# Performance work log

Measured on AMD Instinct MI355X. Metric: run time of the kernel, lower is better.

The kernel has to match this reference:

```python
import jax, jax.numpy as jnp
import numpy as np

N, E, IN_FEATS, HID, CLS, K = 100000, 3200000, 500, 64, 40, 10
EPS = 1e-8

def _col_normalize(x):
    # column-wise L2 norm over nodes (dim=0), clamped at 1e-8
    return x / jnp.clip(jnp.linalg.norm(x, axis=0), EPS, None)

def setup_inputs() -> dict:
    key = jax.random.key(0)
    ks = jax.random.split(key, 9)
    features = jax.random.normal(ks[0], (N, IN_FEATS), jnp.float32)
    noise = jax.random.normal(ks[1], (N, HID), jnp.float32)
    edge_index = jax.random.randint(ks[2], (2, E), 0, N, dtype=jnp.int32)
    norm_A = jax.random.uniform(ks[3], (E,), jnp.float32) * 0.1  # normalized adj weights
    W1 = jax.random.normal(ks[4], (IN_FEATS, HID), jnp.float32) * (1.0 / np.sqrt(IN_FEATS))
    b1 = jax.random.normal(ks[5], (HID,), jnp.float32) * 0.01
    W2 = jax.random.normal(ks[6], (HID, CLS), jnp.float32) * (1.0 / np.sqrt(HID))
    b2 = jax.random.normal(ks[7], (CLS,), jnp.float32) * 0.01
    alpha = jax.random.normal(ks[8], (HID, K + 1), jnp.float32) * 0.1
    return {"features": features, "noise": noise, "norm_A": norm_A, "W1": W1,
            "b1": b1, "W2": W2, "b2": b2, "alpha": alpha, "edge_index": edge_index}

def reference(features, noise, norm_A, W1, b1, W2, b2, alpha, edge_index):
    # fc1 + act (dropout p=0 -> identity)
    x = jax.nn.relu(features @ W1 + b1)
    x = x + noise * 1e-5  # blank_noise = randn_like(x) * 1e-5
    h0 = _col_normalize(x)
    rst = alpha[:, 0] * h0  # broadcast per-channel over nodes
    last_h = h0
    second_last_h = jnp.zeros_like(h0)
    src, dst = edge_index[0], edge_index[1]
    for i in range(1, K + 1):
        # NormalBasisConv: h = A @ last_h (sparse), orthogonalize vs last two, column-normalize
        h = jax.ops.segment_sum(norm_A[:, None] * last_h[src], dst, num_segments=N)  # [N, HID]
        h = h - jnp.sum(h * last_h, axis=0) * last_h
        h = h - jnp.sum(h * second_last_h, axis=0) * second_last_h
        h = _col_normalize(h)
        rst = rst + alpha[:, i] * h
        second_last_h, last_h = last_h, h
    return rst @ W2 + b2
```

## Files before the change

kernel.cpp:

```cpp
#include <hip/hip_runtime.h>
#include <stdint.h>

#define N_NODES 100000
#define N_EDGES 3200000
#define IN_FEATS 500
#define HID 64
#define CLS 40
#define KHOPS 10
#define KT 32
#define NRANGE 8
#define SCAN_BS 256
#define SCAN_NBLK 391

__global__ void zero_kernel(float4* __restrict__ p, size_t n4) {
  size_t i = (size_t)blockIdx.x * blockDim.x + threadIdx.x;
  size_t stride = (size_t)gridDim.x * blockDim.x;
  float4 z = make_float4(0.f, 0.f, 0.f, 0.f);
  for (; i < n4; i += stride) p[i] = z;
}

__global__ void hist_kernel(const int* __restrict__ dst, int* __restrict__ off) {
  const int r = blockIdx.x & (NRANGE - 1);
  const int slice = blockIdx.x >> 3;
  const int nslices = gridDim.x >> 3;
  const int lo = r * (N_NODES / NRANGE);
  const int hi = lo + (N_NODES / NRANGE);
  const int per = (N_EDGES + nslices - 1) / nslices;
  const int beg = slice * per;
  int end = beg + per; if (end > N_EDGES) end = N_EDGES;
  for (int e = beg + threadIdx.x; e < end; e += blockDim.x) {
    int d = dst[e];
    if (d >= lo && d < hi) atomicAdd(&off[d + 1], 1);
  }
}

__launch_bounds__(SCAN_BS)
__global__ void scanA_kernel(const int* __restrict__ off, int* __restrict__ psum) {
  __shared__ int s[SCAN_BS];
  int b = blockIdx.x, t = threadIdx.x;
  int idx = b * SCAN_BS + t;
  s[t] = (idx < N_NODES + 1) ? off[idx] : 0;
  __syncthreads();
  for (int d = SCAN_BS / 2; d > 0; d >>= 1) {
    if (t < d) s[t] += s[t + d];
    __syncthreads();
  }
  if (t == 0) psum[b] = s[0];
}

__launch_bounds__(512)
__global__ void scanB_kernel(int* __restrict__ psum) {
  __shared__ int s[512];
  int t = threadIdx.x;
  s[t] = (t < SCAN_NBLK) ? psum[t] : 0;
  __syncthreads();
  for (int d = 1; d < 512; d <<= 1) {
    int v = (t >= d) ? s[t - d] : 0;
    __syncthreads();
    s[t] += v;
    __syncthreads();
  }
  if (t < SCAN_NBLK) psum[t] = (t == 0) ? 0 : s[t - 1];
}

__launch_bounds__(SCAN_BS)
__global__ void scanC_kernel(int* __restrict__ off, int* __restrict__ cursor,
                             const int* __restrict__ psum) {
  __shared__ int s[SCAN_BS];
  int b = blockIdx.x, t = threadIdx.x;
  int idx = b * SCAN_BS + t;
  s[t] = (idx < N_NODES + 1) ? off[idx] : 0;
  __syncthreads();
  for (int d = 1; d < SCAN_BS; d <<= 1) {
    int v = (t >= d) ? s[t - d] : 0;
    __syncthreads();
    s[t] += v;
    __syncthreads();
  }
  int run = s[t] + psum[b];
  if (idx < N_NODES + 1) {
    off[idx] = run;
    if (idx < N_NODES) cursor[idx] = run;
  }
}

__global__ void fill_kernel(const int* __restrict__ src, const int* __restrict__ dst,
                            const float* __restrict__ w, int* __restrict__ cursor,
                            int2* __restrict__ edges) {
  const int r = blockIdx.x & (NRANGE - 1);
  const int slice = blockIdx.x >> 3;
  const int nslices = gridDim.x >> 3;
  const int lo = r * (N_NODES / NRANGE);
  const int hi = lo + (N_NODES / NRANGE);
  const int per = (N_EDGES + nslices - 1) / nslices;
  const int beg = slice * per;
  int end = beg + per; if (end > N_EDGES) end = N_EDGES;
  for (int e = beg + threadIdx.x; e < end; e += blockDim.x) {
    int d = dst[e];
    if (d >= lo && d < hi) {
      int p = atomicAdd(&cursor[d], 1);
      edges[p] = make_int2(src[e], __float_as_int(w[e]));
    }
  }
}

__launch_bounds__(256)
__global__ void fc1_kernel(const float* __restrict__ F, const float* __restrict__ W1,
                           const float* __restrict__ bias1, const float* __restrict__ noise,
                           float* __restrict__ x, float* __restrict__ nn0) {
  __shared__ float Fs[KT][132];
  __shared__ float Ws[KT][64];
  __shared__ float red[64];
  const int t = threadIdx.x;
  const int tx = t & 15;
  const int ty = t >> 4;
  const int c0 = tx * 4;
  const int n0 = ty * 8;
  const int nodeBase = blockIdx.x * 128;
  const int fk = (t & 7) * 4;
  const int fn = t >> 3;
  const int wr = t >> 3;
  const int wc = (t & 7) * 8;

  float4 fr[4];
  float4 w0r, w1r;
  {
#pragma unroll
    for (int p = 0; p < 4; ++p) {
      int n = nodeBase + fn + 32 * p;
      float4 v = make_float4(0.f, 0.f, 0.f, 0.f);
      if (n < N_NODES && fk + 3 < IN_FEATS) v = *(const float4*)(F + (size_t)n * IN_FEATS + fk);
      fr[p] = v;
    }
    float4 a = make_float4(0.f, 0.f, 0.f, 0.f), b = a;
    if (wr < IN_FEATS) {
      a = *(const float4*)(W1 + (size_t)wr * HID + wc);
      b = *(const float4*)(W1 + (size_t)wr * HID + wc + 4);
    }
    w0r = a; w1r = b;
  }

  float acc[8][4];
#pragma unroll
  for (int i = 0; i < 8; ++i)
#pragma unroll
    for (int j = 0; j < 4; ++j) acc[i][j] = 0.f;

  const int NTILE = (IN_FEATS + KT - 1) / KT;
  for (int tile = 0; tile < NTILE; ++tile) {
    __syncthreads();
#pragma unroll
    for (int p = 0; p < 4; ++p) {
      Fs[fk + 0][fn + 32 * p] = fr[p].x;
      Fs[fk + 1][fn + 32 * p] = fr[p].y;
      Fs[fk + 2][fn + 32 * p] = fr[p].z;
      Fs[fk + 3][fn + 32 * p] = fr[p].w;
    }
    *(float4*)&Ws[wr][wc] = w0r;
    *(float4*)&Ws[wr][wc + 4] = w1r;
    __syncthreads();
    if (tile + 1 < NTILE) {
      const int kb = (tile + 1) * KT;
#pragma unroll
      for (int p = 0; p < 4; ++p) {
        int n = nodeBase + fn + 32 * p;
        int k = kb + fk;
        float4 v = make_float4(0.f, 0.f, 0.f, 0.f);
        if (n < N_NODES && k + 3 < IN_FEATS) v = *(const float4*)(F + (size_t)n * IN_FEATS + k);
        fr[p] = v;
      }
      int k = kb + wr;
      float4 a = make_float4(0.f, 0.f, 0.f, 0.f), b = a;
      if (k < IN_FEATS) {
        a = *(const float4*)(W1 + (size_t)k * HID + wc);
        b = *(const float4*)(W1 + (size_t)k * HID + wc + 4);
      }
      w0r = a; w1r = b;
    }
#pragma unroll 8
    for (int kk = 0; kk < KT; ++kk) {
      float4 fa = *(float4*)&Fs[kk][n0];
      float4 fb = *(float4*)&Fs[kk][n0 + 4];
      float4 wv = *(float4*)&Ws[kk][c0];
      acc[0][0] = fmaf(fa.x, wv.x, acc[0][0]); acc[0][1] = fmaf(fa.x, wv.y, acc[0][1]);
      acc[0][2] = fmaf(fa.x, wv.z, acc[0][2]); acc[0][3] = fmaf(fa.x, wv.w, acc[0][3]);
      acc[1][0] = fmaf(fa.y, wv.x, acc[1][0]); acc[1][1] = fmaf(fa.y, wv.y, acc[1][1]);
      acc[1][2] = fmaf(fa.y, wv.z, acc[1][2]); acc[1][3] = fmaf(fa.y, wv.w, acc[1][3]);
      acc[2][0] = fmaf(fa.z, wv.x, acc[2][0]); acc[2][1] = fmaf(fa.z, wv.y, acc[2][1]);
      acc[2][2] = fmaf(fa.z, wv.z, acc[2][2]); acc[2][3] = fmaf(fa.z, wv.w, acc[2][3]);
      acc[3][0] = fmaf(fa.w, wv.x, acc[3][0]); acc[3][1] = fmaf(fa.w, wv.y, acc[3][1]);
      acc[3][2] = fmaf(fa.w, wv.z, acc[3][2]); acc[3][3] = fmaf(fa.w, wv.w, acc[3][3]);
      acc[4][0] = fmaf(fb.x, wv.x, acc[4][0]); acc[4][1] = fmaf(fb.x, wv.y, acc[4][1]);
      acc[4][2] = fmaf(fb.x, wv.z, acc[4][2]); acc[4][3] = fmaf(fb.x, wv.w, acc[4][3]);
      acc[5][0] = fmaf(fb.y, wv.x, acc[5][0]); acc[5][1] = fmaf(fb.y, wv.y, acc[5][1]);
      acc[5][2] = fmaf(fb.y, wv.z, acc[5][2]); acc[5][3] = fmaf(fb.y, wv.w, acc[5][3]);
      acc[6][0] = fmaf(fb.z, wv.x, acc[6][0]); acc[6][1] = fmaf(fb.z, wv.y, acc[6][1]);
      acc[6][2] = fmaf(fb.z, wv.z, acc[6][2]); acc[6][3] = fmaf(fb.z, wv.w, acc[6][3]);
      acc[7][0] = fmaf(fb.w, wv.x, acc[7][0]); acc[7][1] = fmaf(fb.w, wv.y, acc[7][1]);
      acc[7][2] = fmaf(fb.w, wv.z, acc[7][2]); acc[7][3] = fmaf(fb.w, wv.w, acc[7][3]);
    }
  }

  float4 bb = *(const float4*)(bias1 + c0);
  float np0 = 0.f, np1 = 0.f, np2 = 0.f, np3 = 0.f;
#pragma unroll
  for (int i = 0; i < 8; ++i) {
    int n = nodeBase + n0 + i;
    if (n < N_NODES) {
      float4 nz = *(const float4*)(noise + (size_t)n * HID + c0);
      float v0 = fmaxf(acc[i][0] + bb.x, 0.f) + nz.x * 1e-5f;
      float v1 = fmaxf(acc[i][1] + bb.y, 0.f) + nz.y * 1e-5f;
      float v2 = fmaxf(acc[i][2] + bb.z, 0.f) + nz.z * 1e-5f;
      float v3 = fmaxf(acc[i][3] + bb.w, 0.f) + nz.w * 1e-5f;
      *(float4*)(x + (size_t)n * HID + c0) = make_float4(v0, v1, v2, v3);
      np0 = fmaf(v0, v0, np0); np1 = fmaf(v1, v1, np1);
      np2 = fmaf(v2, v2, np2); np3 = fmaf(v3, v3, np3);
    }
  }
  if (t < 64) red[t] = 0.f;
  __syncthreads();
  atomicAdd(&red[c0 + 0], np0); atomicAdd(&red[c0 + 1], np1);
  atomicAdd(&red[c0 + 2], np2); atomicAdd(&red[c0 + 3], np3);
  __syncthreads();
  if (t < 64) atomicAdd(&nn0[t], red[t]);
}

__launch_bounds__(256)
__global__ void spmm_kernel(const int2* __restrict__ edges, const int* __restrict__ off,
                            const float* __restrict__ lastr, const float* __restrict__ secondr,
                            const float* __restrict__ nn_l,
                            float* __restrict__ h, float* __restrict__ dslot) {
  __shared__ float red[128];
  const int t = threadIdx.x;
  const int lane = t & 63;
  const int wid = __builtin_amdgcn_readfirstlane(t >> 6);
  if (t < 128) red[t] = 0.f;
  __syncthreads();
  const float sig = 1.f / fmaxf(sqrtf(nn_l[lane]), 1e-8f);
  float d1 = 0.f, d2 = 0.f;
  const int nw = gridDim.x * 4;
  for (int n = blockIdx.x * 4 + wid; n < N_NODES; n += nw) {
    const int beg = off[n], end = off[n + 1];
    float a0 = 0.f, a1 = 0.f, a2 = 0.f, a3 = 0.f;
    float a4 = 0.f, a5 = 0.f, a6 = 0.f, a7 = 0.f;
    int j = beg;
    for (; j + 8 <= end; j += 8) {
      int2 e0 = edges[j + 0]; int2 e1 = edges[j + 1];
      int2 e2 = edges[j + 2]; int2 e3 = edges[j + 3];
      int2 e4 = edges[j + 4]; int2 e5 = edges[j + 5];
      int2 e6 = edges[j + 6]; int2 e7 = edges[j + 7];
      a0 = fmaf(__int_as_float(e0.y), lastr[(size_t)e0.x * HID + lane], a0);
      a1 = fmaf(__int_as_float(e1.y), lastr[(size_t)e1.x * HID + lane], a1);
      a2 = fmaf(__int_as_float(e2.y), lastr[(size_t)e2.x * HID + lane], a2);
      a3 = fmaf(__int_as_float(e3.y), lastr[(size_t)e3.x * HID + lane], a3);
      a4 = fmaf(__int_as_float(e4.y), lastr[(size_t)e4.x * HID + lane], a4);
      a5 = fmaf(__int_as_float(e5.y), lastr[(size_t)e5.x * HID + lane], a5);
      a6 = fmaf(__int_as_float(e6.y), lastr[(size_t)e6.x * HID + lane], a6);
      a7 = fmaf(__int_as_float(e7.y), lastr[(size_t)e7.x * HID + lane], a7);
    }
    for (; j < end; ++j) {
      int2 e = edges[j];
      a0 = fmaf(__int_as_float(e.y), lastr[(size_t)e.x * HID + lane], a0);
    }
    float acc = ((a0 + a1) + (a2 + a3)) + ((a4 + a5) + (a6 + a7));
    acc *= sig;
    size_t o = (size_t)n * HID + lane;
    float l = lastr[o], s = secondr[o];
    h[o] = acc;
    d1 = fmaf(acc, l, d1);
    d2 = fmaf(acc, s, d2);
  }
  atomicAdd(&red[lane], d1);
  atomicAdd(&red[64 + lane], d2);
  __syncthreads();
  if (t < 128) atomicAdd(&dslot[t], red[t]);
}

__launch_bounds__(256)
__global__ void passB_kernel(float4* __restrict__ h4, const float4* __restrict__ l4,
                             const float4* __restrict__ s4, float* __restrict__ dcur,
                             const float* __restrict__ nn_l, const float* __restrict__ nn_s,
                             const float* __restrict__ alpha, int prevcol, int accum,
                             float4* __restrict__ rst4) {
  __shared__ float red[64];
  int t = threadIdx.x;
  int q = t & 15;
  int c0 = q * 4;
  float4 NL = ((const float4*)nn_l)[q];
  float4 NS = ((const float4*)nn_s)[q];
  float4 D1 = ((const float4*)dcur)[q];
  float4 D2 = ((const float4*)(dcur + 64))[q];
  float4 sigl, sigs;
  sigl.x = 1.f / fmaxf(sqrtf(NL.x), 1e-8f); sigl.y = 1.f / fmaxf(sqrtf(NL.y), 1e-8f);
  sigl.z = 1.f / fmaxf(sqrtf(NL.z), 1e-8f); sigl.w = 1.f / fmaxf(sqrtf(NL.w), 1e-8f);
  sigs.x = 1.f / fmaxf(sqrtf(NS.x), 1e-8f); sigs.y = 1.f / fmaxf(sqrtf(NS.y), 1e-8f);
  sigs.z = 1.f / fmaxf(sqrtf(NS.z), 1e-8f); sigs.w = 1.f / fmaxf(sqrtf(NS.w), 1e-8f);
  float4 C1, C2, AL;
  C1.x = sigl.x * sigl.x * D1.x; C1.y = sigl.y * sigl.y * D1.y;
  C1.z = sigl.z * sigl.z * D1.z; C1.w = sigl.w * sigl.w * D1.w;
  C2.x = sigs.x * sigs.x * D2.x; C2.y = sigs.y * sigs.y * D2.y;
  C2.z = sigs.z * sigs.z * D2.z; C2.w = sigs.w * sigs.w * D2.w;
  AL.x = alpha[(size_t)(c0 + 0) * (KHOPS + 1) + prevcol] * sigl.x;
  AL.y = alpha[(size_t)(c0 + 1) * (KHOPS + 1) + prevcol] * sigl.y;
  AL.z = alpha[(size_t)(c0 + 2) * (KHOPS + 1) + prevcol] * sigl.z;
  AL.w = alpha[(size_t)(c0 + 3) * (KHOPS + 1) + prevcol] * sigl.w;
  float nx = 0.f, ny = 0.f, nz = 0.f, nw = 0.f;
  int row0 = blockIdx.x * 16 + (t >> 4);
  int rstride = gridDim.x * 16;
  for (int n = row0; n < N_NODES; n += rstride) {
    size_t idx = (size_t)n * 16 + q;
    float4 h = h4[idx];
    float4 l = l4[idx];
    float4 s = s4[idx];
    h.x -= C1.x * l.x + C2.x * s.x;
    h.y -= C1.y * l.y + C2.y * s.y;
    h.z -= C1.z * l.z + C2.z * s.z;
    h.w -= C1.w * l.w + C2.w * s.w;
    h4[idx] = h;
    nx = fmaf(h.x, h.x, nx); ny = fmaf(h.y, h.y, ny);
    nz = fmaf(h.z, h.z, nz); nw = fmaf(h.w, h.w, nw);
    float4 r;
    if (accum) {
      r = rst4[idx];
      r.x = fmaf(AL.x, l.x, r.x); r.y = fmaf(AL.y, l.y, r.y);
      r.z = fmaf(AL.z, l.z, r.z); r.w = fmaf(AL.w, l.w, r.w);
    } else {
      r.x = AL.x * l.x; r.y = AL.y * l.y; r.z = AL.z * l.z; r.w = AL.w * l.w;
    }
    rst4[idx] = r;
  }
  if (t < 64) red[t] = 0.f;
  __syncthreads();
  atomicAdd(&red[c0 + 0], nx); atomicAdd(&red[c0 + 1], ny);
  atomicAdd(&red[c0 + 2], nz); atomicAdd(&red[c0 + 3], nw);
  __syncthreads();
  if (t < 64) atomicAdd(&dcur[128 + t], red[t]);
}

__launch_bounds__(256)
__global__ void gemm2_kernel(const float* __restrict__ rst, const float* __restrict__ hK,
                             const float* __restrict__ nnK, const float* __restrict__ alpha,
                             const float* __restrict__ W2, const float* __restrict__ bias2,
                             float* __restrict__ out) {
  __shared__ float W2s[HID * CLS];
  __shared__ float R[64][65];
  __shared__ float coef[64];
  int t = threadIdx.x;
  if (t < 64) coef[t] = alpha[(size_t)t * (KHOPS + 1) + KHOPS] / fmaxf(sqrtf(nnK[t]), 1e-8f);
  for (int i = t; i < HID * CLS; i += 256) W2s[i] = W2[i];
  int nodeBase = blockIdx.x * 64;
  __syncthreads();
  for (int i = t; i < 64 * 16; i += 256) {
    int r = i >> 4, c4 = (i & 15) * 4;
    int n = nodeBase + r;
    if (n < N_NODES) {
      float4 rv = *(const float4*)(rst + (size_t)n * HID + c4);
      float4 hv = *(const float4*)(hK + (size_t)n * HID + c4);
      R[r][c4 + 0] = rv.x + coef[c4 + 0] * hv.x;
      R[r][c4 + 1] = rv.y + coef[c4 + 1] * hv.y;
      R[r][c4 + 2] = rv.z + coef[c4 + 2] * hv.z;
      R[r][c4 + 3] = rv.w + coef[c4 + 3] * hv.w;
    } else {
      R[r][c4 + 0] = 0.f; R[r][c4 + 1] = 0.f; R[r][c4 + 2] = 0.f; R[r][c4 + 3] = 0.f;
    }
  }
  __syncthreads();
  int node = t >> 2;
  int cls0 = (t & 3) * 10;
  float o[10];
#pragma unroll
  for (int j = 0; j < 10; ++j) o[j] = bias2[cls0 + j];
#pragma unroll 4
  for (int k = 0; k < HID; ++k) {
    float rv = R[node][k];
    const float* wrow = &W2s[k * CLS + cls0];
#pragma unroll
    for (int j = 0; j < 10; ++j) o[j] = fmaf(rv, wrow[j], o[j]);
  }
  int n = nodeBase + node;
  if (n < N_NODES) {
#pragma unroll
    for (int j = 0; j < 10; ++j) out[(size_t)n * CLS + cls0 + j] = o[j];
  }
}

extern "C" void kernel_launch(void* const* d_in, const int* in_sizes, int n_in,
                              void* d_out, int out_size, void* d_ws, size_t ws_size,
                              hipStream_t stream) {
  (void)in_sizes; (void)n_in; (void)out_size;
  const float* features  = (const float*)d_in[0];
  const float* noise     = (const float*)d_in[1];
  const float* norm_A    = (const float*)d_in[2];
  const float* W1        = (const float*)d_in[3];
  const float* b1        = (const float*)d_in[4];
  const float* W2        = (const float*)d_in[5];
  const float* b2        = (const float*)d_in[6];
  const float* alpha     = (const float*)d_in[7];
  const int*   edge_index= (const int*)d_in[8];
  float* out = (float*)d_out;

  char* ws = (char*)d_ws;
  const size_t NB = (size_t)N_NODES * HID * sizeof(float);
  const size_t CURSOR_PAD = 400128;
  float* hA    = (float*)(ws);
  float* hC    = (float*)(ws + NB);
  float* rst   = (float*)(ws + 2 * NB);
  int2*  edges = (int2*)(ws + 3 * NB);
  int*   cursor= (int*)(ws + 4 * NB);
  char*  zbase = ws + 4 * NB + CURSOR_PAD;
  float* hB    = (float*)(zbase);
  int*   off   = (int*)(zbase + NB);
  float* dots  = (float*)(zbase + NB + 400128);
  const size_t zspan = NB + 400128 + (size_t)12 * 192 * 4;
  int*   psum  = (int*)(zbase + zspan);
  const size_t total = 4 * NB + CURSOR_PAD + zspan + 4096;
  if (ws_size < total) return;

  zero_kernel<<<4096, 256, 0, stream>>>((float4*)zbase, zspan / 16);
  hist_kernel<<<2048, 256, 0, stream>>>(edge_index + N_EDGES, off);
  scanA_kernel<<<SCAN_NBLK, SCAN_BS, 0, stream>>>(off, psum);
  scanB_kernel<<<1, 512, 0, stream>>>(psum);
  scanC_kernel<<<SCAN_NBLK, SCAN_BS, 0, stream>>>(off, cursor, psum);
  fill_kernel<<<2048, 256, 0, stream>>>(edge_index, edge_index + N_EDGES, norm_A, cursor, edges);
  fc1_kernel<<<(N_NODES + 127) / 128, 256, 0, stream>>>(features, W1, b1, noise, hA,
                                                        dots + 1 * 192 + 128);
  float* second = hB; float* last = hA; float* cur = hC;
  for (int i = 1; i <= KHOPS; ++i) {
    float* dc = dots + (size_t)(i + 1) * 192;
    float* nl = dots + (size_t)(i)     * 192 + 128;
    float* ns = dots + (size_t)(i - 1) * 192 + 128;
    spmm_kernel<<<2048, 256, 0, stream>>>(edges, off, last, second, nl, cur, dc);
    passB_kernel<<<1024, 256, 0, stream>>>((float4*)cur, (const float4*)last,
                                           (const float4*)second, dc, nl, ns,
                                           alpha, i - 1, (i > 1) ? 1 : 0, (float4*)rst);
    float* tmp = second; second = last; last = cur; cur = tmp;
  }
  gemm2_kernel<<<(N_NODES + 63) / 64, 256, 0, stream>>>(rst, last,
                                                        dots + (size_t)(KHOPS + 1) * 192 + 128,
                                                        alpha, W2, b2, out);
}
```

Before: 2.621 ms.

## Bucket CSR edges by source range and sweep SpMM bucket-by-bucket for cache locality

Builds a two-level CSR keyed by (dst, src>>13), giving 13 source buckets per destination node. The histogram, scan and fill kernels are enlarged to match, and the scan-of-partials is widened to 1024 threads. The SpMM now gives each wave 13 nodes and walks all of them through one source bucket before moving to the next. The goal is to keep the gathered rows of the previous hop inside a roughly 2 MB window at a time, so they are served from L2 instead of the larger last-level cache. In exchange, the inner loop loses its 8-way unrolled independent loads, reads many more offsets, and the preprocessing scan grows. Non-temporal loads and stores and an occupancy hint are added alongside.

Measured after the change: 3.580 ms. 36.6% more time.

```diff
diff --git a/kernel.cpp b/kernel.cpp
--- a/kernel.cpp
+++ b/kernel.cpp
@@ -9,8 +9,14 @@
 #define KHOPS 10
 #define KT 32
 #define NRANGE 8
+#define NBKT 13
+#define BSHIFT 13
+#define NOFF2 (N_NODES * NBKT)
+#define M2 (NOFF2 + 1)
 #define SCAN_BS 256
-#define SCAN_NBLK 391
+#define SCAN_NBLK2 ((M2 + SCAN_BS - 1) / SCAN_BS)
+#define SCANB_T 1024
+#define SCANB_CH ((SCAN_NBLK2 + SCANB_T - 1) / SCANB_T)
 
 __global__ void zero_kernel(float4* __restrict__ p, size_t n4) {
   size_t i = (size_t)blockIdx.x * blockDim.x + threadIdx.x;
@@ -19,7 +25,8 @@
   for (; i < n4; i += stride) p[i] = z;
 }
 
-__global__ void hist_kernel(const int* __restrict__ dst, int* __restrict__ off) {
+__global__ void hist_kernel(const int* __restrict__ src, const int* __restrict__ dst,
+                            int* __restrict__ off2) {
   const int r = blockIdx.x & (NRANGE - 1);
   const int slice = blockIdx.x >> 3;
   const int nslices = gridDim.x >> 3;
@@ -29,17 +36,20 @@
   const int beg = slice * per;
   int end = beg + per; if (end > N_EDGES) end = N_EDGES;
   for (int e = beg + threadIdx.x; e < end; e += blockDim.x) {
-    int d = dst[e];
-    if (d >= lo && d < hi) atomicAdd(&off[d + 1], 1);
+    int d = __builtin_nontemporal_load(dst + e);
+    if (d >= lo && d < hi) {
+      int s = __builtin_nontemporal_load(src + e);
+      atomicAdd(&off2[d * NBKT + (s >> BSHIFT) + 1], 1);
+    }
   }
 }
 
 __launch_bounds__(SCAN_BS)
-__global__ void scanA_kernel(const int* __restrict__ off, int* __restrict__ psum) {
+__global__ void scanA_kernel(const int* __restrict__ off2, int* __restrict__ psum) {
   __shared__ int s[SCAN_BS];
   int b = blockIdx.x, t = threadIdx.x;
   int idx = b * SCAN_BS + t;
-  s[t] = (idx < N_NODES + 1) ? off[idx] : 0;
+  s[t] = (idx < M2) ? off2[idx] : 0;
   __syncthreads();
   for (int d = SCAN_BS / 2; d > 0; d >>= 1) {
     if (t < d) s[t] += s[t + d];
@@ -48,28 +58,42 @@
   if (t == 0) psum[b] = s[0];
 }
 
-__launch_bounds__(512)
+__launch_bounds__(SCANB_T)
 __global__ void scanB_kernel(int* __restrict__ psum) {
-  __shared__ int s[512];
+  __shared__ int s[SCANB_T];
   int t = threadIdx.x;
-  s[t] = (t < SCAN_NBLK) ? psum[t] : 0;
-  __syncthreads();
-  for (int d = 1; d < 512; d <<= 1) {
-    int v = (t >= d) ? s[t - d] : 0;
-    __syncthreads();
-    s[t] += v;
-    __syncthreads();
-  }
-  if (t < SCAN_NBLK) psum[t] = (t == 0) ? 0 : s[t - 1];
+  int base = t * SCANB_CH;
+  int v[SCANB_CH];
+  int sum = 0;
+#pragma unroll
+  for (int k = 0; k < SCANB_CH; ++k) {
+    int i = base + k;
+    v[k] = (i < SCAN_NBLK2) ? psum[i] : 0;
+    sum += v[k];
+  }
+  s[t] = sum;
+  __syncthreads();
+  for (int d = 1; d < SCANB_T; d <<= 1) {
+    int x = (t >= d) ? s[t - d] : 0;
+    __syncthreads();
+    s[t] += x;
+    __syncthreads();
+  }
+  int run = (t == 0) ? 0 : s[t - 1];
+#pragma unroll
+  for (int k = 0; k < SCANB_CH; ++k) {
+    int i = base + k;
+    if (i < SCAN_NBLK2) { psum[i] = run; run += v[k]; }
+  }
 }
 
 __launch_bounds__(SCAN_BS)
-__global__ void scanC_kernel(int* __restrict__ off, int* __restrict__ cursor,
+__global__ void scanC_kernel(int* __restrict__ off2, int* __restrict__ cursor2,
                              const int* __restrict__ psum) {
   __shared__ int s[SCAN_BS];
   int b = blockIdx.x, t = threadIdx.x;
   int idx = b * SCAN_BS + t;
-  s[t] = (idx < N_NODES + 1) ? off[idx] : 0;
+  s[t] = (idx < M2) ? off2[idx] : 0;
   __syncthreads();
   for (int d = 1; d < SCAN_BS; d <<= 1) {
     int v = (t >= d) ? s[t - d] : 0;
@@ -78,14 +102,14 @@
     __syncthreads();
   }
   int run = s[t] + psum[b];
-  if (idx < N_NODES + 1) {
-    off[idx] = run;
-    if (idx < N_NODES) cursor[idx] = run;
+  if (idx < M2) {
+    off2[idx] = run;
+    if (idx < NOFF2) cursor2[idx] = run;
   }
 }
 
 __global__ void fill_kernel(const int* __restrict__ src, const int* __restrict__ dst,
-                            const float* __restrict__ w, int* __restrict__ cursor,
+                            const float* __restrict__ w, int* __restrict__ cursor2,
                             int2* __restrict__ edges) {
   const int r = blockIdx.x & (NRANGE - 1);
   const int slice = blockIdx.x >> 3;
@@ -96,10 +120,12 @@
   const int beg = slice * per;
   int end = beg + per; if (end > N_EDGES) end = N_EDGES;
   for (int e = beg + threadIdx.x; e < end; e += blockDim.x) {
-    int d = dst[e];
+    int d = __builtin_nontemporal_load(dst + e);
     if (d >= lo && d < hi) {
-      int p = atomicAdd(&cursor[d], 1);
-      edges[p] = make_int2(src[e], __float_as_int(w[e]));
+      int s = __builtin_nontemporal_load(src + e);
+      float wv = __builtin_nontemporal_load(w + e);
+      int p = atomicAdd(&cursor2[d * NBKT + (s >> BSHIFT)], 1);
+      edges[p] = make_int2(s, __float_as_int(wv));
     }
   }
 }
@@ -225,8 +251,8 @@
   if (t < 64) atomicAdd(&nn0[t], red[t]);
 }
 
-__launch_bounds__(256)
-__global__ void spmm_kernel(const int2* __restrict__ edges, const int* __restrict__ off,
+__launch_bounds__(256, 8)
+__global__ void spmm_kernel(const int2* __restrict__ edges, const int* __restrict__ off2,
                             const float* __restrict__ lastr, const float* __restrict__ secondr,
                             const float* __restrict__ nn_l,
                             float* __restrict__ h, float* __restrict__ dslot) {
@@ -237,38 +263,45 @@
   if (t < 128) red[t] = 0.f;
   __syncthreads();
   const float sig = 1.f / fmaxf(sqrtf(nn_l[lane]), 1e-8f);
+  const int wg = blockIdx.x * 4 + wid;
+  const unsigned long long* eraw = (const unsigned long long*)edges;
+  float acc[13];
+#pragma unroll
+  for (int d = 0; d < 13; ++d) acc[d] = 0.f;
+
+  for (int b = 0; b < NBKT; ++b) {
+#pragma unroll
+    for (int d = 0; d < 13; ++d) {
+      const int n = wg + d * 8192;
+      if (n < N_NODES) {
+        const size_t kbase = (size_t)n * NBKT + b;
+        const int beg = __builtin_amdgcn_readfirstlane(off2[kbase]);
+        const int end = __builtin_amdgcn_readfirstlane(off2[kbase + 1]);
+        float a = acc[d];
+        for (int j = beg; j < end; ++j) {
+          unsigned long long e = __builtin_nontemporal_load(eraw + j);
+          const int es = (int)(unsigned)(e & 0xffffffffull);
+          const float ew = __int_as_float((int)(unsigned)(e >> 32));
+          a = fmaf(ew, lastr[(size_t)es * HID + lane], a);
+        }
+        acc[d] = a;
+      }
+    }
+  }
+
   float d1 = 0.f, d2 = 0.f;
-  const int nw = gridDim.x * 4;
-  for (int n = blockIdx.x * 4 + wid; n < N_NODES; n += nw) {
-    const int beg = off[n], end = off[n + 1];
-    float a0 = 0.f, a1 = 0.f, a2 = 0.f, a3 = 0.f;
-    float a4 = 0.f, a5 = 0.f, a6 = 0.f, a7 = 0.f;
-    int j = beg;
-    for (; j + 8 <= end; j += 8) {
-      int2 e0 = edges[j + 0]; int2 e1 = edges[j + 1];
-      int2 e2 = edges[j + 2]; int2 e3 = edges[j + 3];
-      int2 e4 = edges[j + 4]; int2 e5 = edges[j + 5];
-      int2 e6 = edges[j + 6]; int2 e7 = edges[j + 7];
-      a0 = fmaf(__int_as_float(e0.y), lastr[(size_t)e0.x * HID + lane], a0);
-      a1 = fmaf(__int_as_float(e1.y), lastr[(size_t)e1.x * HID + lane], a1);
-      a2 = fmaf(__int_as_float(e2.y), lastr[(size_t)e2.x * HID + lane], a2);
-      a3 = fmaf(__int_as_float(e3.y), lastr[(size_t)e3.x * HID + lane], a3);
-      a4 = fmaf(__int_as_float(e4.y), lastr[(size_t)e4.x * HID + lane], a4);
-      a5 = fmaf(__int_as_float(e5.y), lastr[(size_t)e5.x * HID + lane], a5);
-      a6 = fmaf(__int_as_float(e6.y), lastr[(size_t)e6.x * HID + lane], a6);
-      a7 = fmaf(__int_as_float(e7.y), lastr[(size_t)e7.x * HID + lane], a7);
-    }
-    for (; j < end; ++j) {
-      int2 e = edges[j];
-      a0 = fmaf(__int_as_float(e.y), lastr[(size_t)e.x * HID + lane], a0);
-    }
-    float acc = ((a0 + a1) + (a2 + a3)) + ((a4 + a5) + (a6 + a7));
-    acc *= sig;
-    size_t o = (size_t)n * HID + lane;
-    float l = lastr[o], s = secondr[o];
-    h[o] = acc;
-    d1 = fmaf(acc, l, d1);
-    d2 = fmaf(acc, s, d2);
+#pragma unroll
+  for (int d = 0; d < 13; ++d) {
+    const int n = wg + d * 8192;
+    if (n < N_NODES) {
+      size_t o = (size_t)n * HID + lane;
+      float a = acc[d] * sig;
+      float l = lastr[o];
+      float s = __builtin_nontemporal_load(secondr + o);
+      __builtin_nontemporal_store(a, h + o);
+      d1 = fmaf(a, l, d1);
+      d2 = fmaf(a, s, d2);
+    }
   }
   atomicAdd(&red[lane], d1);
   atomicAdd(&red[64 + lane], d2);
@@ -401,27 +434,28 @@
 
   char* ws = (char*)d_ws;
   const size_t NB = (size_t)N_NODES * HID * sizeof(float);
-  const size_t CURSOR_PAD = 400128;
+  const size_t OFF2_BYTES = 5200128;
+  const size_t DOTS_BYTES = (size_t)12 * 192 * 4;
   float* hA    = (float*)(ws);
   float* hC    = (float*)(ws + NB);
   float* rst   = (float*)(ws + 2 * NB);
   int2*  edges = (int2*)(ws + 3 * NB);
-  int*   cursor= (int*)(ws + 4 * NB);
-  char*  zbase = ws + 4 * NB + CURSOR_PAD;
+  char*  zbase = ws + 4 * NB;
   float* hB    = (float*)(zbase);
-  int*   off   = (int*)(zbase + NB);
-  float* dots  = (float*)(zbase + NB + 400128);
-  const size_t zspan = NB + 400128 + (size_t)12 * 192 * 4;
+  int*   off2  = (int*)(zbase + NB);
+  float* dots  = (float*)(zbase + NB + OFF2_BYTES);
+  const size_t zspan = NB + OFF2_BYTES + DOTS_BYTES;
   int*   psum  = (int*)(zbase + zspan);
-  const size_t total = 4 * NB + CURSOR_PAD + zspan + 4096;
+  int*   cursor2 = (int*)rst;
+  const size_t total = 4 * NB + zspan + 20480;
   if (ws_size < total) return;
 
   zero_kernel<<<4096, 256, 0, stream>>>((float4*)zbase, zspan / 16);
-  hist_kernel<<<2048, 256, 0, stream>>>(edge_index + N_EDGES, off);
-  scanA_kernel<<<SCAN_NBLK, SCAN_BS, 0, stream>>>(off, psum);
-  scanB_kernel<<<1, 512, 0, stream>>>(psum);
-  scanC_kernel<<<SCAN_NBLK, SCAN_BS, 0, stream>>>(off, cursor, psum);
-  fill_kernel<<<2048, 256, 0, stream>>>(edge_index, edge_index + N_EDGES, norm_A, cursor, edges);
+  hist_kernel<<<2048, 256, 0, stream>>>(edge_index, edge_index + N_EDGES, off2);
+  scanA_kernel<<<SCAN_NBLK2, SCAN_BS, 0, stream>>>(off2, psum);
+  scanB_kernel<<<1, SCANB_T, 0, stream>>>(psum);
+  scanC_kernel<<<SCAN_NBLK2, SCAN_BS, 0, stream>>>(off2, cursor2, psum);
+  fill_kernel<<<2048, 256, 0, stream>>>(edge_index, edge_index + N_EDGES, norm_A, cursor2, edges);
   fc1_kernel<<<(N_NODES + 127) / 128, 256, 0, stream>>>(features, W1, b1, noise, hA,
                                                         dots + 1 * 192 + 128);
   float* second = hB; float* last = hA; float* cur = hC;
@@ -429,7 +463,7 @@
     float* dc = dots + (size_t)(i + 1) * 192;
     float* nl = dots + (size_t)(i)     * 192 + 128;
     float* ns = dots + (size_t)(i - 1) * 192 + 128;
-    spmm_kernel<<<2048, 256, 0, stream>>>(edges, off, last, second, nl, cur, dc);
+    spmm_kernel<<<2048, 256, 0, stream>>>(edges, off2, last, second, nl, cur, dc);
     passB_kernel<<<1024, 256, 0, stream>>>((float4*)cur, (const float4*)last,
                                            (const float4*)second, dc, nl, ns,
                                            alpha, i - 1, (i > 1) ? 1 : 0, (float4*)rst);
```
